# Kernel tuning notes

Hardware: AMD Instinct MI355X
Metric: run time of the kernel (lower is better)

The kernel has to match this reference:

```python
import jax, jax.numpy as jnp
import numpy as np

PATCH = 16

def setup_inputs() -> dict:
    key = jax.random.key(0)
    k1, k2, k3, k4, k5 = jax.random.split(key, 5)
    B, C, H, W = 128, 3, 224, 224
    N = (H // PATCH) * (W // PATCH)  # 196
    D = 768
    x = jax.random.normal(k1, (B, C, H, W), dtype=jnp.float32)
    ys = jax.random.randint(k2, (B, N), 0, H - PATCH + 1, dtype=jnp.int64)
    xs = jax.random.randint(k3, (B, N), 0, W - PATCH + 1, dtype=jnp.int64)
    W_proj = jax.random.normal(k4, (D, C * PATCH * PATCH), dtype=jnp.float32) * 0.02
    b_proj = jax.random.normal(k5, (D,), dtype=jnp.float32) * 0.02
    return {"x": x, "ys": ys, "xs": xs, "W_proj": W_proj, "b_proj": b_proj}

def reference(x, ys, xs, W_proj, b_proj):
    # x: [B, C, H, W]; ys, xs: [B, N] top-left patch coords
    B, C, H, W = x.shape
    N = ys.shape[1]
    P = PATCH
    # flattened within-patch offsets: d[p] = dy*W + dx, shape [P*P]
    dy = jnp.arange(P)[:, None]
    dx = jnp.arange(P)[None, :]
    d = (dy * W + dx).reshape(-1)  # [P*P]
    base = ys * W + xs                         # [B, N]
    indices = base[:, :, None] + d[None, None, :]  # [B, N, P*P]
    indices = indices.reshape(B, N * P * P)
    # gather over flattened spatial dims for every channel
    x_flat = x.reshape(B, C, H * W)
    patches = jnp.take_along_axis(
        x_flat, indices[:, None, :].astype(jnp.int32), axis=2
    )  # [B, C, N*P*P]
    patches = patches.reshape(B, C, N, P * P)
    patches = patches.transpose(0, 2, 1, 3).reshape(B, N, C * P * P)  # [B, N, C*P*P]
    patch_tokens = jnp.einsum('bnf,df->bnd', patches, W_proj) + b_proj  # [B, N, D]
    patch_positions = jnp.stack([ys, xs], axis=-1)  # [B, N, 2]
    return (patch_tokens, patch_positions)
```

## Files before the change

kernel.cpp:

```cpp
#include <hip/hip_runtime.h>
#include <hip/hip_bf16.h>

#define B_IMG   128
#define CH      3
#define HW      224
#define NPATCH  196
#define TOKENS  25088
#define PATCH   16
#define FDIM    768
#define DDIM    768
#define TOKELEMS ((size_t)TOKENS * FDIM)
#define OUT_TOKENS ((size_t)TOKENS * DDIM)

#define GATHER_BLOCKS (TOKENS * (FDIM / 4) / 256)
#define WCONV_BLOCKS  ((DDIM * FDIM / 4) / 256)

typedef short short8 __attribute__((ext_vector_type(8)));
typedef float f32x4  __attribute__((ext_vector_type(4)));

static __device__ __forceinline__ unsigned short f2bf(float v) {
  unsigned u = __float_as_uint(v);
  unsigned r = u + 0x7fffu + ((u >> 16) & 1u);
  return (unsigned short)(r >> 16);
}

static __device__ __forceinline__ void gload16(const short* g, short* l) {
  __builtin_amdgcn_global_load_lds(
      (const __attribute__((address_space(1))) void*)g,
      (__attribute__((address_space(3))) void*)l,
      16, 0, 0);
}

__global__ __launch_bounds__(256) void prep_kernel(
    const float* __restrict__ x, const int* __restrict__ ys,
    const int* __restrict__ xs, const float* __restrict__ W,
    short* __restrict__ patches, short* __restrict__ Wbf,
    float* __restrict__ pos) {
  const int blk = blockIdx.x;
  if (blk < GATHER_BLOCKS) {
    int e   = blk * 256 + threadIdx.x;
    int tok = e / 192;
    int q   = e - tok * 192;
    int f   = q * 4;
    int b   = tok / NPATCH;
    int y   = ys[tok];
    int xc  = xs[tok];
    int c   = f >> 8;
    int rem = f & 255;
    int py  = rem >> 4;
    int px  = rem & 15;
    const float* src = x + ((size_t)(b * CH + c) * HW + (y + py)) * HW + xc + px;
    ushort4 o;
    o.x = f2bf(src[0]); o.y = f2bf(src[1]); o.z = f2bf(src[2]); o.w = f2bf(src[3]);
    *(ushort4*)&patches[(size_t)tok * FDIM + f] = o;
    if (q == 0) {
      pos[(size_t)tok * 2]     = (float)y;
      pos[(size_t)tok * 2 + 1] = (float)xc;
    }
  } else {
    int i = ((blk - GATHER_BLOCKS) * 256 + threadIdx.x) * 4;
    float4 v = *(const float4*)&W[i];
    ushort4 o;
    o.x = f2bf(v.x); o.y = f2bf(v.y); o.z = f2bf(v.z); o.w = f2bf(v.w);
    *(ushort4*)&Wbf[i] = o;
  }
}

__global__ __launch_bounds__(256) void gemm_kernel(
    const short* __restrict__ A,
    const short* __restrict__ Bw,
    const float* __restrict__ bias,
    float* __restrict__ C) {
  __shared__ short At[2][128 * 32];
  __shared__ short Bt[2][128 * 32];

  const int tid  = threadIdx.x;
  const int w    = tid >> 6;
  const int l    = tid & 63;

  const int id  = blockIdx.x;
  const int nid = (id & 7) * 147 + (id >> 3);
  const int m0  = (nid / 6) * 128;
  const int n0  = (nid % 6) * 128;

  const int wrow = w >> 1;
  const int wcol = w & 1;
  const int lr   = l & 15;
  const int lg   = l >> 4;

  f32x4 acc[4][4];
  const f32x4 z = {0.f, 0.f, 0.f, 0.f};
#pragma unroll
  for (int mi = 0; mi < 4; ++mi)
#pragma unroll
    for (int ni = 0; ni < 4; ++ni) acc[mi][ni] = z;

  const int rw = w * 32;
  const short* gA = A + (size_t)(m0 + rw + (l >> 2)) * FDIM + ((l & 3) << 3);
  const short* gB = Bw + (size_t)(n0 + rw + (l >> 2)) * FDIM + ((l & 3) << 3);
  short* lA0 = &At[0][rw * 32];
  short* lA1 = &At[1][rw * 32];
  short* lB0 = &Bt[0][rw * 32];
  short* lB1 = &Bt[1][rw * 32];

  auto stage = [&](short* lA, short* lB, int ko) {
    gload16(gA + ko, lA);
    gload16(gA + 16 * FDIM + ko, lA + 16 * 32);
    gload16(gB + ko, lB);
    gload16(gB + 16 * FDIM + ko, lB + 16 * 32);
  };
  auto compute = [&](const short* Ab, const short* Bb) {
    short8 a[4], b[4];
    const int koff = lg * 8;
#pragma unroll
    for (int mi = 0; mi < 4; ++mi)
      a[mi] = *(const short8*)&Ab[(wrow * 64 + mi * 16 + lr) * 32 + koff];
#pragma unroll
    for (int ni = 0; ni < 4; ++ni)
      b[ni] = *(const short8*)&Bb[(wcol * 64 + ni * 16 + lr) * 32 + koff];
#pragma unroll
    for (int mi = 0; mi < 4; ++mi)
#pragma unroll
      for (int ni = 0; ni < 4; ++ni)
        acc[mi][ni] =
            __builtin_amdgcn_mfma_f32_16x16x32_bf16(a[mi], b[ni], acc[mi][ni], 0, 0, 0);
  };

  stage(lA0, lB0, 0);
  asm volatile("s_waitcnt vmcnt(0)" ::: "memory");
  __syncthreads();

  for (int kt = 0; kt < 24; kt += 2) {
    stage(lA1, lB1, (kt + 1) * 32);
    compute(At[0], Bt[0]);
    asm volatile("s_waitcnt vmcnt(0)" ::: "memory");
    __syncthreads();
    if (kt + 2 < 24) stage(lA0, lB0, (kt + 2) * 32);
    compute(At[1], Bt[1]);
    asm volatile("s_waitcnt vmcnt(0)" ::: "memory");
    __syncthreads();
  }

#pragma unroll
  for (int ni = 0; ni < 4; ++ni) {
    const int col = n0 + wcol * 64 + ni * 16 + lr;
    const float bs = bias[col];
#pragma unroll
    for (int mi = 0; mi < 4; ++mi) {
      const int row = m0 + wrow * 64 + mi * 16 + lg * 4;
      const f32x4 v = acc[mi][ni];
#pragma unroll
      for (int j = 0; j < 4; ++j)
        C[(size_t)(row + j) * DDIM + col] = v[j] + bs;
    }
  }
}

__global__ __launch_bounds__(256) void naive_kernel(
    const float* __restrict__ x, const int* __restrict__ ys,
    const int* __restrict__ xs, const float* __restrict__ W,
    const float* __restrict__ bias, float* __restrict__ out) {
  __shared__ float prow[FDIM];
  const int tok = blockIdx.x;
  const int t   = threadIdx.x;
  const int b   = tok / NPATCH;
  const int y   = ys[tok];
  const int xc  = xs[tok];
  for (int i = t; i < FDIM; i += 256) {
    int c = i >> 8, rem = i & 255, py = rem >> 4, px = rem & 15;
    prow[i] = x[((size_t)(b * CH + c) * HW + y + py) * HW + xc + px];
  }
  __syncthreads();
  for (int dd = 0; dd < 3; ++dd) {
    const int d = t + dd * 256;
    float s = bias[d];
    const float4* wr = (const float4*)&W[(size_t)d * FDIM];
    const float4* pr = (const float4*)prow;
    for (int f4 = 0; f4 < FDIM / 4; ++f4) {
      float4 wv = wr[f4];
      float4 pv = pr[f4];
      s += wv.x * pv.x + wv.y * pv.y + wv.z * pv.z + wv.w * pv.w;
    }
    out[(size_t)tok * DDIM + d] = s;
  }
  if (t == 0) {
    float* pos = out + OUT_TOKENS;
    pos[(size_t)tok * 2]     = (float)y;
    pos[(size_t)tok * 2 + 1] = (float)xc;
  }
}

extern "C" void kernel_launch(void* const* d_in, const int* in_sizes, int n_in,
                              void* d_out, int out_size, void* d_ws, size_t ws_size,
                              hipStream_t stream) {
  const float* x    = (const float*)d_in[0];
  const int*   ys   = (const int*)d_in[1];
  const int*   xs   = (const int*)d_in[2];
  const float* W    = (const float*)d_in[3];
  const float* bias = (const float*)d_in[4];
  float* out = (float*)d_out;
  float* pos = out + OUT_TOKENS;

  const size_t w_bytes = (size_t)DDIM * FDIM * 2;
  const size_t p_bytes = TOKELEMS * 2;
  if (ws_size >= w_bytes + p_bytes) {
    short* Wbf     = (short*)d_ws;
    short* patches = (short*)d_ws + (size_t)DDIM * FDIM;
    prep_kernel<<<GATHER_BLOCKS + WCONV_BLOCKS, 256, 0, stream>>>(
        x, ys, xs, W, patches, Wbf, pos);
    gemm_kernel<<<(TOKENS / 128) * (DDIM / 128), 256, 0, stream>>>(
        patches, Wbf, bias, out);
  } else {
    naive_kernel<<<TOKENS, 256, 0, stream>>>(x, ys, xs, W, bias, out);
  }
}
```

Measured before the change: 93.01 us.

## Deepen GEMM LDS pipeline to four stages with partial vmcnt waits

```diff
diff --git a/kernel.cpp b/kernel.cpp
--- a/kernel.cpp
+++ b/kernel.cpp
@@ -71,8 +71,8 @@
     const short* __restrict__ Bw,
     const float* __restrict__ bias,
     float* __restrict__ C) {
-  __shared__ short At[2][128 * 32];
-  __shared__ short Bt[2][128 * 32];
+  __shared__ short At[4][128 * 32];
+  __shared__ short Bt[4][128 * 32];
 
   const int tid  = threadIdx.x;
   const int w    = tid >> 6;
@@ -95,21 +95,29 @@
 #pragma unroll
     for (int ni = 0; ni < 4; ++ni) acc[mi][ni] = z;
 
+  float bs[4];
+#pragma unroll
+  for (int ni = 0; ni < 4; ++ni)
+    bs[ni] = bias[n0 + wcol * 64 + ni * 16 + lr];
+#pragma unroll
+  for (int ni = 0; ni < 4; ++ni) asm volatile("" : "+v"(bs[ni]));
+
   const int rw = w * 32;
   const short* gA = A + (size_t)(m0 + rw + (l >> 2)) * FDIM + ((l & 3) << 3);
   const short* gB = Bw + (size_t)(n0 + rw + (l >> 2)) * FDIM + ((l & 3) << 3);
-  short* lA0 = &At[0][rw * 32];
-  short* lA1 = &At[1][rw * 32];
-  short* lB0 = &Bt[0][rw * 32];
-  short* lB1 = &Bt[1][rw * 32];
-
-  auto stage = [&](short* lA, short* lB, int ko) {
+
+  auto stage = [&](int buf, int kt) {
+    const int ko = kt * 32;
+    short* lA = &At[buf][rw * 32];
+    short* lB = &Bt[buf][rw * 32];
     gload16(gA + ko, lA);
     gload16(gA + 16 * FDIM + ko, lA + 16 * 32);
     gload16(gB + ko, lB);
     gload16(gB + 16 * FDIM + ko, lB + 16 * 32);
   };
-  auto compute = [&](const short* Ab, const short* Bb) {
+  auto compute = [&](int buf) {
+    const short* Ab = At[buf];
+    const short* Bb = Bt[buf];
     short8 a[4], b[4];
     const int koff = lg * 8;
 #pragma unroll
@@ -118,40 +126,49 @@
 #pragma unroll
     for (int ni = 0; ni < 4; ++ni)
       b[ni] = *(const short8*)&Bb[(wcol * 64 + ni * 16 + lr) * 32 + koff];
+    __builtin_amdgcn_s_setprio(1);
 #pragma unroll
     for (int mi = 0; mi < 4; ++mi)
 #pragma unroll
       for (int ni = 0; ni < 4; ++ni)
         acc[mi][ni] =
             __builtin_amdgcn_mfma_f32_16x16x32_bf16(a[mi], b[ni], acc[mi][ni], 0, 0, 0);
+    __builtin_amdgcn_s_setprio(0);
   };
 
-  stage(lA0, lB0, 0);
+  stage(0, 0);
+  stage(1, 1);
+  stage(2, 2);
+
+  for (int t = 0; t < 21; ++t) {
+    stage((t + 3) & 3, t + 3);
+    asm volatile("s_waitcnt vmcnt(12)" ::: "memory");
+    __builtin_amdgcn_s_barrier();
+    compute(t & 3);
+    __builtin_amdgcn_s_barrier();
+  }
+  asm volatile("s_waitcnt vmcnt(8)" ::: "memory");
+  __builtin_amdgcn_s_barrier();
+  compute(21 & 3);
+  __builtin_amdgcn_s_barrier();
+  asm volatile("s_waitcnt vmcnt(4)" ::: "memory");
+  __builtin_amdgcn_s_barrier();
+  compute(22 & 3);
+  __builtin_amdgcn_s_barrier();
   asm volatile("s_waitcnt vmcnt(0)" ::: "memory");
-  __syncthreads();
-
-  for (int kt = 0; kt < 24; kt += 2) {
-    stage(lA1, lB1, (kt + 1) * 32);
-    compute(At[0], Bt[0]);
-    asm volatile("s_waitcnt vmcnt(0)" ::: "memory");
-    __syncthreads();
-    if (kt + 2 < 24) stage(lA0, lB0, (kt + 2) * 32);
-    compute(At[1], Bt[1]);
-    asm volatile("s_waitcnt vmcnt(0)" ::: "memory");
-    __syncthreads();
-  }
+  __builtin_amdgcn_s_barrier();
+  compute(23 & 3);
 
 #pragma unroll
   for (int ni = 0; ni < 4; ++ni) {
     const int col = n0 + wcol * 64 + ni * 16 + lr;
-    const float bs = bias[col];
 #pragma unroll
     for (int mi = 0; mi < 4; ++mi) {
       const int row = m0 + wrow * 64 + mi * 16 + lg * 4;
       const f32x4 v = acc[mi][ni];
 #pragma unroll
       for (int j = 0; j < 4; ++j)
-        C[(size_t)(row + j) * DDIM + col] = v[j] + bs;
+        C[(size_t)(row + j) * DDIM + col] = v[j] + bs[ni];
     }
   }
 }
```

Result: faster. 89.94 us (-3.3%).

## Replace LDS-staged block GEMM with per-wave register-direct 64x64 tiles

Applied to the files above, without the earlier changes.

```diff
diff --git a/kernel.cpp b/kernel.cpp
--- a/kernel.cpp
+++ b/kernel.cpp
@@ -22,13 +22,6 @@
   unsigned u = __float_as_uint(v);
   unsigned r = u + 0x7fffu + ((u >> 16) & 1u);
   return (unsigned short)(r >> 16);
-}
-
-static __device__ __forceinline__ void gload16(const short* g, short* l) {
-  __builtin_amdgcn_global_load_lds(
-      (const __attribute__((address_space(1))) void*)g,
-      (__attribute__((address_space(3))) void*)l,
-      16, 0, 0);
 }
 
 __global__ __launch_bounds__(256) void prep_kernel(
@@ -71,22 +64,26 @@
     const short* __restrict__ Bw,
     const float* __restrict__ bias,
     float* __restrict__ C) {
-  __shared__ short At[2][128 * 32];
-  __shared__ short Bt[2][128 * 32];
-
-  const int tid  = threadIdx.x;
-  const int w    = tid >> 6;
-  const int l    = tid & 63;
+  const int tid = threadIdx.x;
+  const int w   = tid >> 6;
+  const int l   = tid & 63;
+  const int lr  = l & 15;
+  const int lg  = l >> 4;
 
   const int id  = blockIdx.x;
   const int nid = (id & 7) * 147 + (id >> 3);
-  const int m0  = (nid / 6) * 128;
-  const int n0  = (nid % 6) * 128;
+  const int job = nid * 4 + w;
+  const int mt  = job / 12;
+  const int nt  = job - mt * 12;
+  const int m0  = mt * 64;
+  const int n0  = nt * 64;
 
-  const int wrow = w >> 1;
-  const int wcol = w & 1;
-  const int lr   = l & 15;
-  const int lg   = l >> 4;
+  const short* gA = A  + (size_t)(m0 + lr) * FDIM + lg * 8;
+  const short* gB = Bw + (size_t)(n0 + lr) * FDIM + lg * 8;
+
+  float bs[4];
+#pragma unroll
+  for (int ni = 0; ni < 4; ++ni) bs[ni] = bias[n0 + ni * 16 + lr];
 
   f32x4 acc[4][4];
   const f32x4 z = {0.f, 0.f, 0.f, 0.f};
@@ -95,65 +92,51 @@
 #pragma unroll
     for (int ni = 0; ni < 4; ++ni) acc[mi][ni] = z;
 
-  const int rw = w * 32;
-  const short* gA = A + (size_t)(m0 + rw + (l >> 2)) * FDIM + ((l & 3) << 3);
-  const short* gB = Bw + (size_t)(n0 + rw + (l >> 2)) * FDIM + ((l & 3) << 3);
-  short* lA0 = &At[0][rw * 32];
-  short* lA1 = &At[1][rw * 32];
-  short* lB0 = &Bt[0][rw * 32];
-  short* lB1 = &Bt[1][rw * 32];
+  short8 A0[4], B0[4], A1[4], B1[4];
 
-  auto stage = [&](short* lA, short* lB, int ko) {
-    gload16(gA + ko, lA);
-    gload16(gA + 16 * FDIM + ko, lA + 16 * 32);
-    gload16(gB + ko, lB);
-    gload16(gB + 16 * FDIM + ko, lB + 16 * 32);
-  };
-  auto compute = [&](const short* Ab, const short* Bb) {
-    short8 a[4], b[4];
-    const int koff = lg * 8;
-#pragma unroll
-    for (int mi = 0; mi < 4; ++mi)
-      a[mi] = *(const short8*)&Ab[(wrow * 64 + mi * 16 + lr) * 32 + koff];
-#pragma unroll
-    for (int ni = 0; ni < 4; ++ni)
-      b[ni] = *(const short8*)&Bb[(wcol * 64 + ni * 16 + lr) * 32 + koff];
-#pragma unroll
-    for (int mi = 0; mi < 4; ++mi)
-#pragma unroll
-      for (int ni = 0; ni < 4; ++ni)
-        acc[mi][ni] =
-            __builtin_amdgcn_mfma_f32_16x16x32_bf16(a[mi], b[ni], acc[mi][ni], 0, 0, 0);
-  };
+#define LOADSET(Af, Bf, kt)                                                  \
+  do {                                                                       \
+    const short* pa = gA + (kt) * 32;                                        \
+    const short* pb = gB + (kt) * 32;                                        \
+    _Pragma("unroll")                                                        \
+    for (int i = 0; i < 4; ++i) Af[i] = *(const short8*)(pa + i * 16 * FDIM);\
+    _Pragma("unroll")                                                        \
+    for (int i = 0; i < 4; ++i) Bf[i] = *(const short8*)(pb + i * 16 * FDIM);\
+  } while (0)
 
-  stage(lA0, lB0, 0);
-  asm volatile("s_waitcnt vmcnt(0)" ::: "memory");
-  __syncthreads();
+#define MFMASET(Af, Bf)                                                      \
+  do {                                                                       \
+    _Pragma("unroll")                                                        \
+    for (int mi = 0; mi < 4; ++mi)                                           \
+      _Pragma("unroll")                                                      \
+      for (int ni = 0; ni < 4; ++ni)                                         \
+        acc[mi][ni] = __builtin_amdgcn_mfma_f32_16x16x32_bf16(               \
+            Af[mi], Bf[ni], acc[mi][ni], 0, 0, 0);                           \
+  } while (0)
 
+  LOADSET(A0, B0, 0);
   for (int kt = 0; kt < 24; kt += 2) {
-    stage(lA1, lB1, (kt + 1) * 32);
-    compute(At[0], Bt[0]);
-    asm volatile("s_waitcnt vmcnt(0)" ::: "memory");
-    __syncthreads();
-    if (kt + 2 < 24) stage(lA0, lB0, (kt + 2) * 32);
-    compute(At[1], Bt[1]);
-    asm volatile("s_waitcnt vmcnt(0)" ::: "memory");
-    __syncthreads();
+    LOADSET(A1, B1, kt + 1);
+    MFMASET(A0, B0);
+    const int k2 = (kt + 2 < 24) ? kt + 2 : 0;
+    LOADSET(A0, B0, k2);
+    MFMASET(A1, B1);
   }
 
 #pragma unroll
   for (int ni = 0; ni < 4; ++ni) {
-    const int col = n0 + wcol * 64 + ni * 16 + lr;
-    const float bs = bias[col];
+    const int col = n0 + ni * 16 + lr;
 #pragma unroll
     for (int mi = 0; mi < 4; ++mi) {
-      const int row = m0 + wrow * 64 + mi * 16 + lg * 4;
+      const int row = m0 + mi * 16 + lg * 4;
       const f32x4 v = acc[mi][ni];
 #pragma unroll
       for (int j = 0; j < 4; ++j)
-        C[(size_t)(row + j) * DDIM + col] = v[j] + bs;
+        C[(size_t)(row + j) * DDIM + col] = v[j] + bs[ni];
     }
   }
+#undef LOADSET
+#undef MFMASET
 }
 
 __global__ __launch_bounds__(256) void naive_kernel(
@@ -208,7 +191,7 @@
     short* patches = (short*)d_ws + (size_t)DDIM * FDIM;
     prep_kernel<<<GATHER_BLOCKS + WCONV_BLOCKS, 256, 0, stream>>>(
         x, ys, xs, W, patches, Wbf, pos);
-    gemm_kernel<<<(TOKENS / 128) * (DDIM / 128), 256, 0, stream>>>(
+    gemm_kernel<<<(TOKENS / 64 / 4) * (DDIM / 64), 256, 0, stream>>>(
         patches, Wbf, bias, out);
   } else {
     naive_kernel<<<TOKENS, 256, 0, stream>>>(x, ys, xs, W, bias, out);
```

Result: slower. 151.2 us (+62.5%).
